# Performance work log

Hardware: AMD Instinct MI355X
Metric: run time of the kernel (lower is better)

## Reference

```python
import math
import jax, jax.numpy as jnp
import numpy as np

_GELU_C = math.sqrt(2.0 / math.pi)

def _gelu_tanh(x):
    return 0.5 * x * (1.0 + jnp.tanh(_GELU_C * (x + 0.044715 * x * x * x)))

def _l2_normalize(v, eps=1e-12):
    # matches F.normalize: v / max(||v||, eps)
    n = jnp.sqrt(jnp.sum(v * v, axis=-1, keepdims=True))
    return v / jnp.maximum(n, eps)

def setup_inputs() -> dict:
    key = jax.random.key(0)
    k1, k2, k3 = jax.random.split(key, 3)
    B, T, D = 8, 2048, 1024
    x = jax.random.normal(k1, (B, T, D), dtype=jnp.float32)
    # nn.Parameter initial values from the module
    log_alpha = jnp.asarray(math.log(math.exp(0.5) - 1.0), dtype=jnp.float32)
    log_sigma = jnp.asarray(math.log(1.0), dtype=jnp.float32)
    return {"x": x, "log_alpha": log_alpha, "log_sigma": log_sigma}

def reference(x, log_alpha, log_sigma):
    B, T, D = x.shape
    alpha = jax.nn.softplus(log_alpha)
    sigma = jax.nn.softplus(log_sigma)
    scale = 1.0 / math.sqrt(D)
    # full strictly-past causal attention (triu with diagonal=0 masks self too)
    sim = jnp.einsum('btd,bsd->bts', x, x) * scale            # [B,T,T]
    causal = jnp.triu(jnp.ones((T, T), dtype=bool), k=0)      # True = masked
    sim = jnp.where(causal[None], -jnp.inf, sim)
    # NaN-safe masked softmax: fully-masked rows (t=0) -> all zeros,
    # matching torch softmax + nan_to_num(nan=0.0)
    m = jnp.max(sim, axis=-1, keepdims=True)
    m_safe = jnp.where(jnp.isfinite(m), m, 0.0)
    e = jnp.exp(sim - m_safe)                                 # -inf -> 0
    denom = jnp.sum(e, axis=-1, keepdims=True)
    attn = jnp.where(denom > 0, e / jnp.where(denom > 0, denom, 1.0), 0.0)
    context = jnp.einsum('bts,bsd->btd', attn, x)             # [B,T,D]
    cos_sim = jnp.sum(_l2_normalize(x) * _l2_normalize(context), axis=-1)  # [B,T]
    novelty = jnp.clip(1.0 - cos_sim, 0.0, 2.0) / 2.0
    novelty = jnp.nan_to_num(novelty, nan=1.0)
    gate = 1.0 + alpha * jnp.tanh(sigma * novelty[..., None])
    return _gelu_tanh(x * gate)
```

## Files before the change

kernel.cpp:

```cpp
#include <hip/hip_runtime.h>
#include <math.h>

#define TN 2048
#define DN 1024

typedef __attribute__((ext_vector_type(8))) _Float16 half8;
typedef __attribute__((ext_vector_type(4))) _Float16 half4v;
typedef __attribute__((ext_vector_type(4))) float f32x4;

__device__ __forceinline__ f32x4 mfma16(half8 a, half8 b, f32x4 c) {
  return __builtin_amdgcn_mfma_f32_16x16x32_f16(a, b, c, 0, 0, 0);
}

#define BAR_LDS()  asm volatile("s_waitcnt lgkmcnt(0)\ns_barrier" ::: "memory")
#define WAITVM0()  asm volatile("s_waitcnt vmcnt(0)" ::: "memory")

__device__ __forceinline__ int img_off(int key, int f) {
  const int kg = key >> 2;
  const int p  = ((kg & 1) << 2) | (kg >> 1);
  return (f >> 4) * 512 + p * 64 + (key & 3) * 16 + (f & 15);
}

__global__ __launch_bounds__(256) void convert_x(const float* __restrict__ x,
                                                 _Float16* __restrict__ w) {
  const long long gid = (long long)blockIdx.x * 256 + threadIdx.x;
  const long long e   = gid * 8;
  const int bt   = (int)(e >> 15);
  const int et   = (int)(e & 32767);
  const int f16b = et >> 9;
  const int p    = (et >> 6) & 7;
  const int row  = (et >> 4) & 3;
  const int col0 = et & 15;
  const int kg   = ((p & 3) << 1) | (p >> 2);
  const int key  = kg * 4 + row;
  const size_t xoff = ((size_t)bt * 32 + key) * DN + f16b * 16 + col0;
  float4 u0 = *(const float4*)(x + xoff);
  float4 u1 = *(const float4*)(x + xoff + 4);
  half8 h = {(_Float16)u0.x, (_Float16)u0.y, (_Float16)u0.z, (_Float16)u0.w,
             (_Float16)u1.x, (_Float16)u1.y, (_Float16)u1.z, (_Float16)u1.w};
  *(half8*)(w + e) = h;
}

#define ISSUE4(T, O0, O1, O2, O3)                                             \
  asm volatile("ds_read_b64_tr_b16 %0, %4 offset:" O0 "\n\t"                  \
               "ds_read_b64_tr_b16 %1, %4 offset:" O1 "\n\t"                  \
               "ds_read_b64_tr_b16 %2, %4 offset:" O2 "\n\t"                  \
               "ds_read_b64_tr_b16 %3, %4 offset:" O3                         \
               : "=&v"(T[0]), "=&v"(T[1]), "=&v"(T[2]), "=&v"(T[3])           \
               : "v"(ab));

#define MFMA2(T, CT0, CT1)                                                    \
  {                                                                           \
    half8 bf0 = __builtin_shufflevector(T[0], T[1], 0, 1, 2, 3, 4, 5, 6, 7);  \
    half8 bf1 = __builtin_shufflevector(T[2], T[3], 0, 1, 2, 3, 4, 5, 6, 7);  \
    oacc[CT0] = mfma16(aP, bf0, oacc[CT0]);                                   \
    oacc[CT1] = mfma16(aP, bf1, oacc[CT1]);                                   \
  }

template <bool WS>
__global__ __launch_bounds__(512, 4)
void attn_gate(const float* __restrict__ x, const _Float16* __restrict__ wsx,
               const float* __restrict__ pla, const float* __restrict__ pls,
               float* __restrict__ out) {
  __shared__ _Float16 Kbuf[32768];
  __shared__ _Float16 Sred[8][16][44];
  __shared__ float l_s[16], gate_s[16];

  const int tid = threadIdx.x;
  const int w   = tid >> 6;
  const int l   = tid & 63;
  const int lr  = l & 15;
  const int lg  = l >> 4;
  const int kq  = w;

  const int b   = blockIdx.x & 7;
  const int q16 = 127 - (blockIdx.x >> 3);
  const int qbase = q16 * 16;
  const int nkt   = (qbase + 14) / 32 + 1;

  const float alpha = log1pf(expf(pla[0]));
  const float sigma = log1pf(expf(pls[0]));

  const float* xb = x + (size_t)b * TN * DN;
  float*       ob = out + (size_t)b * TN * DN;

  const int kg0 = lr >> 2;
  const int bk0 = ((((kg0 & 1) << 2) | (kg0 >> 1)) << 6) + (lr & 3) * 16 + (lg & 1) * 8;
  const int kg1 = 4 + (lr >> 2);
  const int bk1 = ((((kg1 & 1) << 2) | (kg1 >> 1)) << 6) + (lr & 3) * 16 + (lg & 1) * 8;

  const _Float16* wsb = WS ? (wsx + (size_t)b * 64 * 32768) : nullptr;

  auto STAGE = [&](int t) {
    if constexpr (WS) {
      const _Float16* tn = wsb + (size_t)t * 32768;
#pragma unroll
      for (int i = 0; i < 8; ++i)
        __builtin_amdgcn_global_load_lds(
            (const __attribute__((address_space(1))) void*)(tn + w * 4096 + i * 512 + l * 8),
            (__attribute__((address_space(3))) void*)(&Kbuf[w * 4096 + i * 512]), 16, 0, 0);
    } else {
      const int skey = tid >> 4, sc = tid & 15;
      const float* kp = xb + (size_t)(t * 32 + skey) * DN + sc * 4;
#pragma unroll
      for (int j = 0; j < 16; ++j) {
        const int f = sc * 4 + 64 * j;
        float4 v = *(const float4*)(kp + 64 * j);
        half4v h = {(_Float16)v.x, (_Float16)v.y, (_Float16)v.z, (_Float16)v.w};
        *(half4v*)&Kbuf[img_off(skey, f)] = h;
      }
    }
  };

  STAGE(0);

  half8 qf[4];
  if constexpr (WS) {
    const _Float16* qtile = wsb + (size_t)(q16 >> 1) * 32768;
    const int qrow = (q16 & 1) * 16 + lr;
    const int g0   = qrow >> 2;
    const int qp   = (((g0 & 1) << 2) | (g0 >> 1)) * 64 + (qrow & 3) * 16 + (lg & 1) * 8;
#pragma unroll
    for (int s = 0; s < 4; ++s)
      qf[s] = *(const half8*)&qtile[(kq * 8 + s * 2 + (lg >> 1)) * 512 + qp];
  } else {
#pragma unroll
    for (int s = 0; s < 4; ++s) {
      const float* qp = xb + (size_t)(qbase + lr) * DN + kq * 128 + s * 32 + lg * 8;
      float4 a = ((const float4*)qp)[0];
      float4 c = ((const float4*)qp)[1];
      half8 h;
      h[0]=(_Float16)a.x; h[1]=(_Float16)a.y; h[2]=(_Float16)a.z; h[3]=(_Float16)a.w;
      h[4]=(_Float16)c.x; h[5]=(_Float16)c.y; h[6]=(_Float16)c.z; h[7]=(_Float16)c.w;
      qf[s] = h;
    }
  }

  f32x4 oacc[8];
#pragma unroll
  for (int ct = 0; ct < 8; ++ct) oacc[ct] = f32x4{0.f, 0.f, 0.f, 0.f};
  float l0 = 0.0f;

  if constexpr (!WS) __syncthreads();

  for (int t = 0; t < nkt; ++t) {
    if constexpr (WS) WAITVM0();

    {
      f32x4 sA = f32x4{0.f,0.f,0.f,0.f};
      f32x4 sB = f32x4{0.f,0.f,0.f,0.f};
      if constexpr (WS) {
        const _Float16* tp = wsb + (size_t)t * 32768;
        half8 af0[4], af1[4];
#pragma unroll
        for (int s = 0; s < 4; ++s) {
          const int base = (kq * 8 + s * 2 + (lg >> 1)) * 512;
          af0[s] = *(const half8*)&tp[base + bk0];
          af1[s] = *(const half8*)&tp[base + bk1];
        }
#pragma unroll
        for (int s = 0; s < 4; ++s) {
          sA = mfma16(af0[s], qf[s], sA);
          sB = mfma16(af1[s], qf[s], sB);
        }
      } else {
#pragma unroll
        for (int s = 0; s < 4; ++s) {
          const int base = (kq * 8 + s * 2 + (lg >> 1)) * 512;
          half8 bf0 = *(const half8*)&Kbuf[base + bk0];
          half8 bf1 = *(const half8*)&Kbuf[base + bk1];
          sA = mfma16(bf0, qf[s], sA);
          sB = mfma16(bf1, qf[s], sB);
        }
      }
      half4v hA = {(_Float16)sA[0], (_Float16)sA[1], (_Float16)sA[2], (_Float16)sA[3]};
      half4v hB = {(_Float16)sB[0], (_Float16)sB[1], (_Float16)sB[2], (_Float16)sB[3]};
      *(half4v*)&Sred[kq][lr][lg * 4]      = hA;
      *(half4v*)&Sred[kq][lr][16 + lg * 4] = hB;
    }
    BAR_LDS();

    {
      half8 r0 = *(const half8*)&Sred[0][lr][lg * 8];
      half8 r1 = *(const half8*)&Sred[1][lr][lg * 8];
      half8 r2 = *(const half8*)&Sred[2][lr][lg * 8];
      half8 r3 = *(const half8*)&Sred[3][lr][lg * 8];
      half8 r4 = *(const half8*)&Sred[4][lr][lg * 8];
      half8 r5 = *(const half8*)&Sred[5][lr][lg * 8];
      half8 r6 = *(const half8*)&Sred[6][lr][lg * 8];
      half8 r7 = *(const half8*)&Sred[7][lr][lg * 8];
      half8 sum = ((r0 + r1) + (r2 + r3)) + ((r4 + r5) + (r6 + r7));

      const bool mt = (t == nkt - 1);
      const int  gb = 32 * t + lg * 8;
      half8 aP;
#pragma unroll
      for (int j = 0; j < 8; ++j) {
        float p = __expf((float)sum[j] * 0.03125f);
        if (mt && (gb + j >= qbase + lr)) p = 0.0f;
        l0 += p;
        aP[j] = (_Float16)p;
      }

      const uint32_t ab = (uint32_t)(uintptr_t)(void*)&Kbuf[w * 4096 + l * 4];
      asm volatile("s_waitcnt lgkmcnt(0)" ::: "memory");
      __builtin_amdgcn_sched_barrier(0);
      half4v t0[4], t1[4];
      ISSUE4(t0, "0", "512", "1024", "1536");
      ISSUE4(t1, "2048", "2560", "3072", "3584");
      asm volatile("s_waitcnt lgkmcnt(4)" ::: "memory");
      __builtin_amdgcn_sched_barrier(0);
      MFMA2(t0, 0, 1);
      ISSUE4(t0, "4096", "4608", "5120", "5632");
      asm volatile("s_waitcnt lgkmcnt(4)" ::: "memory");
      __builtin_amdgcn_sched_barrier(0);
      MFMA2(t1, 2, 3);
      ISSUE4(t1, "6144", "6656", "7168", "7680");
      asm volatile("s_waitcnt lgkmcnt(4)" ::: "memory");
      __builtin_amdgcn_sched_barrier(0);
      MFMA2(t0, 4, 5);
      asm volatile("s_waitcnt lgkmcnt(0)" ::: "memory");
      __builtin_amdgcn_sched_barrier(0);
      MFMA2(t1, 6, 7);
    }

    if (t + 1 < nkt) {
      if constexpr (!WS) __syncthreads();
      STAGE(t + 1);
    }
    BAR_LDS();
  }

  {
    float lt = l0 + __shfl_xor(l0, 16);
    lt += __shfl_xor(lt, 32);
    if (w == 0 && lg == 0) l_s[lr] = lt;
  }

  {
    float* ered = (float*)&Sred[0][0][0];
#pragma unroll
    for (int j = 0; j < 4; ++j) {
      const int row = lg * 4 + j;
      const float* xr = xb + (size_t)(qbase + row) * DN + w * 128 + lr;
      float a1 = 0.f, a2 = 0.f, a3 = 0.f;
#pragma unroll
      for (int ct = 0; ct < 8; ++ct) {
        const float xv = xr[ct * 16];
        const float ov = oacc[ct][j];
        a1 += xv * ov; a2 += xv * xv; a3 += ov * ov;
      }
#pragma unroll
      for (int d = 1; d < 16; d <<= 1) {
        a1 += __shfl_xor(a1, d);
        a2 += __shfl_xor(a2, d);
        a3 += __shfl_xor(a3, d);
      }
      if (lr == 0) {
        float* e = ered + (row * 8 + w) * 4;
        e[0] = a1; e[1] = a2; e[2] = a3;
      }
    }
  }
  __syncthreads();
  if (tid < 16) {
    const float* ered = (const float*)&Sred[0][0][0];
    float SxO = 0.f, Sxx = 0.f, SOO = 0.f;
#pragma unroll
    for (int wv = 0; wv < 8; ++wv) {
      const float* e = ered + (tid * 8 + wv) * 4;
      SxO += e[0]; Sxx += e[1]; SOO += e[2];
    }
    const float lden = l_s[tid];
    float cosv = 0.0f;
    if (lden > 0.0f) {
      const float nx = fmaxf(sqrtf(Sxx), 1e-12f);
      const float nc = fmaxf(sqrtf(SOO) / lden, 1e-12f);
      cosv = (SxO / lden) / (nx * nc);
    }
    float nov = fminf(fmaxf(1.0f - cosv, 0.0f), 2.0f) * 0.5f;
    gate_s[tid] = 1.0f + alpha * tanhf(sigma * nov);
  }
  __syncthreads();
  {
#pragma unroll
    for (int j = 0; j < 4; ++j) {
      const int row = lg * 4 + j;
      const float g = gate_s[row];
      const float* xr = xb + (size_t)(qbase + row) * DN + w * 128 + lr;
      float* orow     = ob + (size_t)(qbase + row) * DN + w * 128 + lr;
#pragma unroll
      for (int ct = 0; ct < 8; ++ct) {
        const float z = xr[ct * 16] * g;
        const float u = 0.7978845608028654f * (z + 0.044715f * z * z * z);
        orow[ct * 16] = 0.5f * z * (1.0f + tanhf(u));
      }
    }
  }
}

extern "C" void kernel_launch(void* const* d_in, const int* in_sizes, int n_in,
                              void* d_out, int out_size, void* d_ws, size_t ws_size,
                              hipStream_t stream) {
  const float* x  = (const float*)d_in[0];
  const float* la = (const float*)d_in[1];
  const float* ls = (const float*)d_in[2];
  float* out = (float*)d_out;
  const size_t need = (size_t)8 * 64 * 32768 * 2;
  if (ws_size >= need) {
    convert_x<<<dim3(8192), dim3(256), 0, stream>>>(x, (_Float16*)d_ws);
    attn_gate<true><<<dim3(1024), dim3(512), 0, stream>>>(
        x, (const _Float16*)d_ws, la, ls, out);
  } else {
    attn_gate<false><<<dim3(1024), dim3(512), 0, stream>>>(
        x, (const _Float16*)nullptr, la, ls, out);
  }
}
```

Measured before the change: 229.0 us.

## Add transposed fp16 V workspace and LDS-free attention kernel with register prefetch

Adds a convert_xt kernel that writes a transposed fp16 copy of x, so the PV MFMA B-operand can be loaded straight from global memory. A new attn_gate2 kernel then reads K fragments and V fragments directly from global into registers, prefetching the next K tile while the current one is used, and drops the LDS staging and transposed LDS reads. This removes LDS traffic and the global-to-LDS copy wait per tile, at the cost of an extra conversion pass over x, twice the workspace, and heavier global and L2 traffic per block. The new path runs when the workspace is large enough; the old kernels remain as fallbacks.

```diff
diff --git a/kernel.cpp b/kernel.cpp
--- a/kernel.cpp
+++ b/kernel.cpp
@@ -41,6 +41,230 @@
   *(half8*)(w + e) = h;
 }
 
+__global__ __launch_bounds__(256) void convert_xt(const float* __restrict__ x,
+                                                  _Float16* __restrict__ vt) {
+  __shared__ float tile[64][65];
+  const int blk = blockIdx.x;
+  const int ft  = blk & 15;
+  const int kt  = (blk >> 4) & 31;
+  const int b   = blk >> 9;
+  const int tid = threadIdx.x;
+#pragma unroll
+  for (int s = 0; s < 4; ++s) {
+    const int r  = (tid >> 4) + s * 16;
+    const int c4 = tid & 15;
+    float4 v = *(const float4*)(x + ((size_t)(b * TN + kt * 64 + r)) * DN +
+                                ft * 64 + c4 * 4);
+    tile[r][c4 * 4 + 0] = v.x; tile[r][c4 * 4 + 1] = v.y;
+    tile[r][c4 * 4 + 2] = v.z; tile[r][c4 * 4 + 3] = v.w;
+  }
+  __syncthreads();
+#pragma unroll
+  for (int s = 0; s < 2; ++s) {
+    const int fr = (tid >> 3) + s * 32;
+    const int kc = tid & 7;
+    half8 h;
+#pragma unroll
+    for (int j = 0; j < 8; ++j) h[j] = (_Float16)tile[kc * 8 + j][fr];
+    *(half8*)(vt + ((size_t)b * DN + ft * 64 + fr) * TN + kt * 64 + kc * 8) = h;
+  }
+}
+
+__global__ __launch_bounds__(512, 4)
+void attn_gate2(const float* __restrict__ x, const _Float16* __restrict__ wsk,
+                const _Float16* __restrict__ wsv,
+                const float* __restrict__ pla, const float* __restrict__ pls,
+                float* __restrict__ out) {
+  __shared__ _Float16 Sred[8][16][44];
+  __shared__ float l_s[16], gate_s[16];
+
+  const int tid = threadIdx.x;
+  const int w   = tid >> 6;
+  const int l   = tid & 63;
+  const int lr  = l & 15;
+  const int lg  = l >> 4;
+  const int kq  = w;
+
+  const int b   = blockIdx.x & 7;
+  const int q16 = 127 - (blockIdx.x >> 3);
+  const int qbase = q16 * 16;
+  const int nkt   = (qbase + 14) / 32 + 1;
+
+  const float alpha = log1pf(expf(pla[0]));
+  const float sigma = log1pf(expf(pls[0]));
+
+  const float* xb = x + (size_t)b * TN * DN;
+  float*       ob = out + (size_t)b * TN * DN;
+
+  const _Float16* kb_img = wsk + (size_t)b * 64 * 32768;
+  const _Float16* vtb    = wsv + (size_t)b * DN * TN;
+
+  const int kg0 = lr >> 2;
+  const int bk0 = ((((kg0 & 1) << 2) | (kg0 >> 1)) << 6) + (lr & 3) * 16 + (lg & 1) * 8;
+  const int kg1 = 4 + (lr >> 2);
+  const int bk1 = ((((kg1 & 1) << 2) | (kg1 >> 1)) << 6) + (lr & 3) * 16 + (lg & 1) * 8;
+
+  half8 qf[4];
+  {
+    const _Float16* qtile = kb_img + (size_t)(q16 >> 1) * 32768;
+    const int qrow = (q16 & 1) * 16 + lr;
+    const int g0   = qrow >> 2;
+    const int qp   = (((g0 & 1) << 2) | (g0 >> 1)) * 64 + (qrow & 3) * 16 + (lg & 1) * 8;
+#pragma unroll
+    for (int s = 0; s < 4; ++s)
+      qf[s] = *(const half8*)&qtile[(kq * 8 + s * 2 + (lg >> 1)) * 512 + qp];
+  }
+
+  const _Float16* vrow0 = vtb + (size_t)(w * 128 + lr) * TN + lg * 8;
+
+  f32x4 oacc[8];
+#pragma unroll
+  for (int ct = 0; ct < 8; ++ct) oacc[ct] = f32x4{0.f, 0.f, 0.f, 0.f};
+  float l0 = 0.0f;
+
+  half8 af0[4], af1[4];
+#pragma unroll
+  for (int s = 0; s < 4; ++s) {
+    const int base = (kq * 8 + s * 2 + (lg >> 1)) * 512;
+    af0[s] = *(const half8*)&kb_img[base + bk0];
+    af1[s] = *(const half8*)&kb_img[base + bk1];
+  }
+
+  for (int t = 0; t < nkt; ++t) {
+    half8 bfvA[4];
+#pragma unroll
+    for (int ct = 0; ct < 4; ++ct)
+      bfvA[ct] = *(const half8*)&vrow0[(size_t)(ct * 16) * TN + 32 * t];
+
+    f32x4 sA = f32x4{0.f,0.f,0.f,0.f};
+    f32x4 sB = f32x4{0.f,0.f,0.f,0.f};
+#pragma unroll
+    for (int s = 0; s < 4; ++s) {
+      sA = mfma16(af0[s], qf[s], sA);
+      sB = mfma16(af1[s], qf[s], sB);
+    }
+
+    half8 bfvB[4];
+#pragma unroll
+    for (int ct = 0; ct < 4; ++ct)
+      bfvB[ct] = *(const half8*)&vrow0[(size_t)((4 + ct) * 16) * TN + 32 * t];
+    if (t + 1 < nkt) {
+      const _Float16* tp = kb_img + (size_t)(t + 1) * 32768;
+#pragma unroll
+      for (int s = 0; s < 4; ++s) {
+        const int base = (kq * 8 + s * 2 + (lg >> 1)) * 512;
+        af0[s] = *(const half8*)&tp[base + bk0];
+        af1[s] = *(const half8*)&tp[base + bk1];
+      }
+    }
+
+    {
+      half4v hA = {(_Float16)sA[0], (_Float16)sA[1], (_Float16)sA[2], (_Float16)sA[3]};
+      half4v hB = {(_Float16)sB[0], (_Float16)sB[1], (_Float16)sB[2], (_Float16)sB[3]};
+      *(half4v*)&Sred[kq][lr][lg * 4]      = hA;
+      *(half4v*)&Sred[kq][lr][16 + lg * 4] = hB;
+    }
+    BAR_LDS();
+
+    {
+      half8 sum = *(const half8*)&Sred[0][lr][lg * 8];
+      sum = sum + *(const half8*)&Sred[1][lr][lg * 8];
+      sum = sum + *(const half8*)&Sred[2][lr][lg * 8];
+      sum = sum + *(const half8*)&Sred[3][lr][lg * 8];
+      sum = sum + *(const half8*)&Sred[4][lr][lg * 8];
+      sum = sum + *(const half8*)&Sred[5][lr][lg * 8];
+      sum = sum + *(const half8*)&Sred[6][lr][lg * 8];
+      sum = sum + *(const half8*)&Sred[7][lr][lg * 8];
+
+      const bool mt = (t == nkt - 1);
+      const int  gb = 32 * t + lg * 8;
+      half8 aP;
+#pragma unroll
+      for (int j = 0; j < 8; ++j) {
+        float p = __expf((float)sum[j] * 0.03125f);
+        if (mt && (gb + j >= qbase + lr)) p = 0.0f;
+        l0 += p;
+        aP[j] = (_Float16)p;
+      }
+
+#pragma unroll
+      for (int ct = 0; ct < 4; ++ct)
+        oacc[ct] = mfma16(aP, bfvA[ct], oacc[ct]);
+#pragma unroll
+      for (int ct = 0; ct < 4; ++ct)
+        oacc[4 + ct] = mfma16(aP, bfvB[ct], oacc[4 + ct]);
+    }
+    BAR_LDS();
+  }
+
+  {
+    float lt = l0 + __shfl_xor(l0, 16);
+    lt += __shfl_xor(lt, 32);
+    if (w == 0 && lg == 0) l_s[lr] = lt;
+  }
+
+  {
+    float* ered = (float*)&Sred[0][0][0];
+#pragma unroll
+    for (int j = 0; j < 4; ++j) {
+      const int row = lg * 4 + j;
+      const float* xr = xb + (size_t)(qbase + row) * DN + w * 128 + lr;
+      float a1 = 0.f, a2 = 0.f, a3 = 0.f;
+#pragma unroll
+      for (int ct = 0; ct < 8; ++ct) {
+        const float xv = xr[ct * 16];
+        const float ov = oacc[ct][j];
+        a1 += xv * ov; a2 += xv * xv; a3 += ov * ov;
+      }
+#pragma unroll
+      for (int d = 1; d < 16; d <<= 1) {
+        a1 += __shfl_xor(a1, d);
+        a2 += __shfl_xor(a2, d);
+        a3 += __shfl_xor(a3, d);
+      }
+      if (lr == 0) {
+        float* e = ered + (row * 8 + w) * 4;
+        e[0] = a1; e[1] = a2; e[2] = a3;
+      }
+    }
+  }
+  __syncthreads();
+  if (tid < 16) {
+    const float* ered = (const float*)&Sred[0][0][0];
+    float SxO = 0.f, Sxx = 0.f, SOO = 0.f;
+#pragma unroll
+    for (int wv = 0; wv < 8; ++wv) {
+      const float* e = ered + (tid * 8 + wv) * 4;
+      SxO += e[0]; Sxx += e[1]; SOO += e[2];
+    }
+    const float lden = l_s[tid];
+    float cosv = 0.0f;
+    if (lden > 0.0f) {
+      const float nx = fmaxf(sqrtf(Sxx), 1e-12f);
+      const float nc = fmaxf(sqrtf(SOO) / lden, 1e-12f);
+      cosv = (SxO / lden) / (nx * nc);
+    }
+    float nov = fminf(fmaxf(1.0f - cosv, 0.0f), 2.0f) * 0.5f;
+    gate_s[tid] = 1.0f + alpha * tanhf(sigma * nov);
+  }
+  __syncthreads();
+  {
+#pragma unroll
+    for (int j = 0; j < 4; ++j) {
+      const int row = lg * 4 + j;
+      const float g = gate_s[row];
+      const float* xr = xb + (size_t)(qbase + row) * DN + w * 128 + lr;
+      float* orow     = ob + (size_t)(qbase + row) * DN + w * 128 + lr;
+#pragma unroll
+      for (int ct = 0; ct < 8; ++ct) {
+        const float z = xr[ct * 16] * g;
+        const float u = 0.7978845608028654f * (z + 0.044715f * z * z * z);
+        orow[ct * 16] = 0.5f * z * (1.0f + tanhf(u));
+      }
+    }
+  }
+}
+
 #define ISSUE4(T, O0, O1, O2, O3)                                             \
   asm volatile("ds_read_b64_tr_b16 %0, %4 offset:" O0 "\n\t"                  \
                "ds_read_b64_tr_b16 %1, %4 offset:" O1 "\n\t"                  \
@@ -89,11 +313,9 @@
   const int kg1 = 4 + (lr >> 2);
   const int bk1 = ((((kg1 & 1) << 2) | (kg1 >> 1)) << 6) + (lr & 3) * 16 + (lg & 1) * 8;
 
-  const _Float16* wsb = WS ? (wsx + (size_t)b * 64 * 32768) : nullptr;
-
   auto STAGE = [&](int t) {
     if constexpr (WS) {
-      const _Float16* tn = wsb + (size_t)t * 32768;
+      const _Float16* tn = wsx + (size_t)(b * 64 + t) * 32768;
 #pragma unroll
       for (int i = 0; i < 8; ++i)
         __builtin_amdgcn_global_load_lds(
@@ -116,7 +338,7 @@
 
   half8 qf[4];
   if constexpr (WS) {
-    const _Float16* qtile = wsb + (size_t)(q16 >> 1) * 32768;
+    const _Float16* qtile = wsx + (size_t)(b * 64 + (q16 >> 1)) * 32768;
     const int qrow = (q16 & 1) * 16 + lr;
     const int g0   = qrow >> 2;
     const int qp   = (((g0 & 1) << 2) | (g0 >> 1)) * 64 + (qrow & 3) * 16 + (lg & 1) * 8;
@@ -149,29 +371,13 @@
     {
       f32x4 sA = f32x4{0.f,0.f,0.f,0.f};
       f32x4 sB = f32x4{0.f,0.f,0.f,0.f};
-      if constexpr (WS) {
-        const _Float16* tp = wsb + (size_t)t * 32768;
-        half8 af0[4], af1[4];
-#pragma unroll
-        for (int s = 0; s < 4; ++s) {
-          const int base = (kq * 8 + s * 2 + (lg >> 1)) * 512;
-          af0[s] = *(const half8*)&tp[base + bk0];
-          af1[s] = *(const half8*)&tp[base + bk1];
-        }
-#pragma unroll
-        for (int s = 0; s < 4; ++s) {
-          sA = mfma16(af0[s], qf[s], sA);
-          sB = mfma16(af1[s], qf[s], sB);
-        }
-      } else {
-#pragma unroll
-        for (int s = 0; s < 4; ++s) {
-          const int base = (kq * 8 + s * 2 + (lg >> 1)) * 512;
-          half8 bf0 = *(const half8*)&Kbuf[base + bk0];
-          half8 bf1 = *(const half8*)&Kbuf[base + bk1];
-          sA = mfma16(bf0, qf[s], sA);
-          sB = mfma16(bf1, qf[s], sB);
-        }
+#pragma unroll
+      for (int s = 0; s < 4; ++s) {
+        const int base = (kq * 8 + s * 2 + (lg >> 1)) * 512;
+        half8 bf0 = *(const half8*)&Kbuf[base + bk0];
+        half8 bf1 = *(const half8*)&Kbuf[base + bk1];
+        sA = mfma16(bf0, qf[s], sA);
+        sB = mfma16(bf1, qf[s], sB);
       }
       half4v hA = {(_Float16)sA[0], (_Float16)sA[1], (_Float16)sA[2], (_Float16)sA[3]};
       half4v hB = {(_Float16)sB[0], (_Float16)sB[1], (_Float16)sB[2], (_Float16)sB[3]};
@@ -181,15 +387,14 @@
     BAR_LDS();
 
     {
-      half8 r0 = *(const half8*)&Sred[0][lr][lg * 8];
-      half8 r1 = *(const half8*)&Sred[1][lr][lg * 8];
-      half8 r2 = *(const half8*)&Sred[2][lr][lg * 8];
-      half8 r3 = *(const half8*)&Sred[3][lr][lg * 8];
-      half8 r4 = *(const half8*)&Sred[4][lr][lg * 8];
-      half8 r5 = *(const half8*)&Sred[5][lr][lg * 8];
-      half8 r6 = *(const half8*)&Sred[6][lr][lg * 8];
-      half8 r7 = *(const half8*)&Sred[7][lr][lg * 8];
-      half8 sum = ((r0 + r1) + (r2 + r3)) + ((r4 + r5) + (r6 + r7));
+      half8 sum = *(const half8*)&Sred[0][lr][lg * 8];
+      sum = sum + *(const half8*)&Sred[1][lr][lg * 8];
+      sum = sum + *(const half8*)&Sred[2][lr][lg * 8];
+      sum = sum + *(const half8*)&Sred[3][lr][lg * 8];
+      sum = sum + *(const half8*)&Sred[4][lr][lg * 8];
+      sum = sum + *(const half8*)&Sred[5][lr][lg * 8];
+      sum = sum + *(const half8*)&Sred[6][lr][lg * 8];
+      sum = sum + *(const half8*)&Sred[7][lr][lg * 8];
 
       const bool mt = (t == nkt - 1);
       const int  gb = 32 * t + lg * 8;
@@ -306,8 +511,15 @@
   const float* la = (const float*)d_in[1];
   const float* ls = (const float*)d_in[2];
   float* out = (float*)d_out;
-  const size_t need = (size_t)8 * 64 * 32768 * 2;
-  if (ws_size >= need) {
+  const size_t needK = (size_t)8 * 64 * 32768 * 2;
+  const size_t needV = (size_t)8 * DN * TN * 2;
+  if (ws_size >= needK + needV) {
+    _Float16* wsk = (_Float16*)d_ws;
+    _Float16* wsv = (_Float16*)((char*)d_ws + needK);
+    convert_x<<<dim3(8192), dim3(256), 0, stream>>>(x, wsk);
+    convert_xt<<<dim3(4096), dim3(256), 0, stream>>>(x, wsv);
+    attn_gate2<<<dim3(1024), dim3(512), 0, stream>>>(x, wsk, wsv, la, ls, out);
+  } else if (ws_size >= needK) {
     convert_x<<<dim3(8192), dim3(256), 0, stream>>>(x, (_Float16*)d_ws);
     attn_gate<true><<<dim3(1024), dim3(512), 0, stream>>>(
         x, (const _Float16*)d_ws, la, ls, out);
```

Result: slower. 902.0 us (+293.9%).
